# Optimization experiments

Hardware: AMD Instinct MI355X
Metric: run time of the kernel (lower is better)

Reference implementation:

```python
import jax, jax.numpy as jnp
import numpy as np

SC = 19          # window stride/size (non-kitti)
K = 3 * SC       # 57, unfold kernel size
CH = 128         # chnn

def conv2d(x, w, b=None, pad=(0, 0)):
    y = jax.lax.conv_general_dilated(
        x, w, (1, 1), [(pad[0], pad[0]), (pad[1], pad[1])],
        dimension_numbers=('NCHW', 'OIHW', 'NCHW'))
    return y if b is None else y + b[None, :, None, None]

def unfold(x):
    # nn.Unfold(kernel_size=3*SC, padding=SC, stride=SC) -> [b, c, K*K, h_sc*w_sc]
    b, c, h, w = x.shape
    h_sc, w_sc = h // SC, w // SC
    xp = jnp.pad(x, ((0, 0), (0, 0), (SC, SC), (SC, SC)))
    ii = np.arange(h_sc)[:, None] * SC + np.arange(K)[None, :]
    jj = np.arange(w_sc)[:, None] * SC + np.arange(K)[None, :]
    p = xp[:, :, ii, :][:, :, :, :, jj]              # [b,c,h_sc,K,w_sc,K]
    return p.transpose(0, 1, 3, 5, 2, 4).reshape(b, c, K * K, h_sc * w_sc)

def to_windows(x):
    # [b,c,h,w] -> [b,c,h_sc*w_sc, SC*SC] (non-overlapping SCxSC windows)
    b, c, h, w = x.shape
    h_sc, w_sc = h // SC, w // SC
    return x.reshape(b, c, h_sc, SC, w_sc, SC).transpose(0, 1, 2, 4, 3, 5).reshape(b, c, h_sc * w_sc, SC * SC)

def fs_kernel(w_prelu, b, h, w):
    # geometric falloff kernel, separable in x/y: [b, K*K, L, SC*SC]
    a = w_prelu[0] * 0.02      # scp = 0.02
    half = 2.0 * SC            # half_ker
    crd = jnp.arange(K, dtype=jnp.float32)
    idx_x = SC + jnp.arange(w, dtype=jnp.float32) % SC
    idx_y = SC + jnp.arange(h, dtype=jnp.float32) % SC
    def falloff(d):
        v = d - half
        pre = jnp.where(v > 0, v, a * v)   # PReLU
        return jnp.maximum(1.0 - pre, 0.0) # -prelu + b(=1), clamped at 0
    ox = falloff(jnp.abs(crd[:, None] - idx_x[None, :]))  # [K, w]
    oy = falloff(jnp.abs(crd[:, None] - idx_y[None, :]))  # [K, h]
    ker = oy[:, None, :, None] * ox[None, :, None, :]      # [Ky, Kx, h, w]
    ker = jnp.broadcast_to(ker[None], (b, K, K, h, w)).reshape(b, K * K, h, w)
    return to_windows(ker)

def kpa(feat_ci, feat_mi, w_qk, w_v, gamma, w_prelu):
    b, c, h_in, w_in = feat_mi.shape
    x_pad = SC - w_in % SC
    y_pad = SC - h_in % SC
    pad4 = ((0, 0), (0, 0), (0, y_pad), (0, x_pad))
    feat_c = jnp.pad(feat_ci, pad4)
    feat_m = jnp.pad(feat_mi, pad4)
    h, w = h_in + y_pad, w_in + x_pad
    h_sc, w_sc = h // SC, w // SC
    # validity mask -> additive -99 bias for padded keys/queries
    fm = jnp.pad(jnp.ones((1, 1, h_in, w_in), feat_mi.dtype), pad4)
    fm_k = unfold(fm)                                  # [1,1,K^2,L]
    fm_q = to_windows(fm)                              # [1,1,L,SC^2]
    am = (fm_k[:, 0, :, :, None] * fm_q[:, 0, None, :, :] - 1.0) * 99.0
    # itr == 0 path: compute attention
    qk = conv2d(feat_c, w_qk)
    feat_q, feat_k = qk[:, :c], qk[:, c:]
    feat_k = unfold(feat_k) * (c ** -0.5)              # [b,c,K^2,L]
    feat_q = to_windows(feat_q)                        # [b,c,L,SC^2]
    attn = jnp.einsum('bckn,bcns->bkns', feat_k, feat_q) + am
    attn = jax.nn.softmax(fs_kernel(w_prelu, b, h, w) * attn, axis=1)
    feat_v = unfold(conv2d(feat_m, w_v))               # [b,c,K^2,L]
    feat_r = jnp.einsum('bkns,bckn->bcns', attn, feat_v)  # [b,c,L,SC^2]
    feat_r = feat_r.reshape(b, c, h_sc, w_sc, SC, SC).transpose(0, 1, 2, 4, 3, 5).reshape(b, c, h, w)
    return feat_mi + feat_r[:, :, :h_in, :w_in] * gamma[0]

def sep_conv_gru(h, x, wz1, bz1, wr1, br1, wq1, bq1, wz2, bz2, wr2, br2, wq2, bq2):
    hx = jnp.concatenate([h, x], 1)
    z = jax.nn.sigmoid(conv2d(hx, wz1, bz1, (0, 2)))
    r = jax.nn.sigmoid(conv2d(hx, wr1, br1, (0, 2)))
    q = jnp.tanh(conv2d(jnp.concatenate([r * h, x], 1), wq1, bq1, (0, 2)))
    h = (1 - z) * h + z * q
    hx = jnp.concatenate([h, x], 1)
    z = jax.nn.sigmoid(conv2d(hx, wz2, bz2, (2, 0)))
    r = jax.nn.sigmoid(conv2d(hx, wr2, br2, (2, 0)))
    q = jnp.tanh(conv2d(jnp.concatenate([r * h, x], 1), wq2, bq2, (2, 0)))
    return (1 - z) * h + z * q

PARAM_SHAPES = [
    ('w_cor1', (256, 324, 1, 1)), ('b_cor1', (256,)), ('w_cor2', (192, 256, 3, 3)), ('b_cor2', (192,)),
    ('w_flo1', (128, 2, 7, 7)), ('b_flo1', (128,)), ('w_flo2', (64, 128, 3, 3)), ('b_flo2', (64,)),
    ('w_mo', (126, 256, 3, 3)), ('b_mo', (126,)),
    ('w_qk', (256, 128, 1, 1)), ('w_v', (128, 128, 1, 1)),
    ('wz1', (128, 512, 1, 5)), ('bz1', (128,)), ('wr1', (128, 512, 1, 5)), ('br1', (128,)),
    ('wq1', (128, 512, 1, 5)), ('bq1', (128,)),
    ('wz2', (128, 512, 5, 1)), ('bz2', (128,)), ('wr2', (128, 512, 5, 1)), ('br2', (128,)),
    ('wq2', (128, 512, 5, 1)), ('bq2', (128,)),
    ('w_f1', (256, 128, 3, 3)), ('b_f1', (256,)), ('w_f2', (2, 256, 3, 3)), ('b_f2', (2,)),
    ('w_m1', (256, 128, 3, 3)), ('b_m1', (256,)), ('w_m2', (576, 256, 1, 1)), ('b_m2', (576,)),
]

def setup_inputs() -> dict:
    key = jax.random.key(0)
    B, H, W = 2, 55, 128
    ks = jax.random.split(key, len(PARAM_SHAPES) + 4)
    inp = {
        'net': jax.random.normal(ks[0], (B, CH, H, W), jnp.float32),
        'inp': jax.random.normal(ks[1], (B, CH, H, W), jnp.float32),
        'corr': jax.random.normal(ks[2], (B, 324, H, W), jnp.float32),
        'flow': jax.random.normal(ks[3], (B, 2, H, W), jnp.float32),
    }
    for i, (name, shp) in enumerate(PARAM_SHAPES):
        fan_in = int(np.prod(shp[1:])) if len(shp) > 1 else shp[0]
        scale = 1.0 / np.sqrt(fan_in) if len(shp) > 1 else 0.01
        inp[name] = scale * jax.random.normal(ks[4 + i], shp, jnp.float32)
    inp['gamma'] = jnp.array([0.5], jnp.float32)            # nonzero so KPA contributes
    inp['w_prelu'] = jnp.array([1.0 / 28.0], jnp.float32)    # 1 / h_k, h_k = (3*SC-1)/2
    inp['itr'] = 0
    return inp

def reference(net, inp, corr, flow, w_cor1, b_cor1, w_cor2, b_cor2, w_flo1, b_flo1, w_flo2, b_flo2, w_mo, b_mo, w_qk, w_v, wz1, bz1, wr1, br1, wq1, bq1, wz2, bz2, wr2, br2, wq2, bq2, w_f1, b_f1, w_f2, b_f2, w_m1, b_m1, w_m2, b_m2, gamma, w_prelu, itr):
    # _mo_enc
    fc = jax.nn.relu(conv2d(corr, w_cor1, b_cor1))
    fc = jax.nn.relu(conv2d(fc, w_cor2, b_cor2, (1, 1)))
    ff = jax.nn.relu(conv2d(flow, w_flo1, b_flo1, (3, 3)))
    ff = jax.nn.relu(conv2d(ff, w_flo2, b_flo2, (1, 1)))
    fm = jax.nn.relu(conv2d(jnp.concatenate([fc, ff], 1), w_mo, b_mo, (1, 1)))
    feat_mo = jnp.concatenate([fm, flow], 1)           # [b,128,h,w]
    # KPA attention (itr == 0)
    feat_moa = kpa(inp, feat_mo, w_qk, w_v, gamma, w_prelu)
    x = jnp.concatenate([inp, feat_mo, feat_moa], 1)   # [b,384,h,w]
    net = sep_conv_gru(net, x, wz1, bz1, wr1, br1, wq1, bq1, wz2, bz2, wr2, br2, wq2, bq2)
    d = jax.nn.relu(conv2d(net, w_f1, b_f1, (1, 1)))
    delta_flow = conv2d(d, w_f2, b_f2, (1, 1))
    m = jax.nn.relu(conv2d(net, w_m1, b_m1, (1, 1)))
    mask = 0.25 * conv2d(m, w_m2, b_m2)
    return net, mask, delta_flow
```

## Files before the change

kernel.cpp:

```cpp
#include <hip/hip_runtime.h>
#include <hip/hip_bf16.h>

typedef __bf16 bf16;
typedef __attribute__((ext_vector_type(8))) __bf16 v8bf;
typedef __attribute__((ext_vector_type(4))) float f32x4;
typedef __attribute__((ext_vector_type(16))) float f32x16;

#define HH 55
#define WW 128
#define HWP 7040
#define BHW 14080
#define QS 0.08838834764831845f
#define LOG2E 1.4426950408889634f

__device__ __forceinline__ void g2l16(const bf16* g, bf16* l){
  __builtin_amdgcn_global_load_lds(
      (const __attribute__((address_space(1))) void*)g,
      (__attribute__((address_space(3))) void*)l, 16, 0, 0);
}

#define NCV 19
__device__ const int PK_srcCS[NCV]  = {324,256,128,256,128,128,512,512,512,512,512,512,128,128,256,256,98,512,512};
__device__ const int PK_csv[NCV]    = {324,256,128,256,128,128,512,512,128,512,512,128,128,128,256,256,98,384,384};
__device__ const int PK_srcOff[NCV] = {0,0,0,0,0,0,0,0,0,0,0,0,0,0,0,0,0,128,128};
__device__ const int PK_wsrc[NCV]   = {0,1,2,3,4,5,6,7,8,9,10,11,12,13,14,15,16,8,11};
__device__ const int PK_Kc[NCV]     = {384,256,128,256,128,128,512,512,128,512,512,128,128,128,256,256,128,384,384};
__device__ const int PK_ntap[NCV]   = {1,9,9,9,1,1,5,5,5,5,5,5,9,9,9,1,1,5,5};
__device__ const int PK_Ctot[NCV]   = {256,256,128,128,256,128,256,256,128,256,256,128,512,512,128,640,128,128,128};
__device__ const int PK_coB[NCV]    = {0,0,0,0,0,0,0,128,0,0,128,0,0,256,0,0,0,0,0};
__device__ const int PK_dst[NCV]    = {0,98304,688128,835584,1130496,1163264,1179648,1179648,
  1835008,2162688,2162688,2818048,3145728,3145728,3735552,4030464,4194304,1916928,2899968};
__device__ const int PKD_cum[NCV+1] = {0,98304,540672,614400,904704,937472,953856,
  1281536,1609216,1691136,2018816,2346496,2428416,2723328,3018240,3022848,3170304,
  3186688,3432448,3678208};
__device__ const int PKD_Co[NCV]    = {256,192,64,126,256,128,128,128,128,128,128,128,256,256,2,576,128,128,128};

__device__ const int PB_off[15]={0,256,512,640,1152,1280,1408,1536,1664,1792,1920,2176,2432,2560,3200};
__device__ const int PB_cnt[15]={256,192,64,126,128,128,128,128,128,128,256,256,2,576,128};

struct W17 { const float* w[17]; };
struct B15 { const float* b[15]; };

struct XP {
  W17 wp; B15 bp;
  const float *net, *inp, *corr, *flow;
  bf16 *Bp; float *bias;
  bf16 *hx; float *hcur; bf16 *corr_cl; bf16 *im2c;
};

__global__ __launch_bounds__(256) void init_k(XP X){
  __shared__ float T[64][65];
  int bid = blockIdx.x;
  const int t = threadIdx.x;
  if (bid < 14368){
    int idx = bid*256 + t;
    int c = 0;
    while (idx >= PKD_cum[c+1]) ++c;
    int local = idx - PKD_cum[c];
    if (c == 16){
      int co = local >> 7, k = local & 127;
      if (k < 98)
        X.Bp[PK_dst[16] + co*128 + k] = (bf16)X.wp.w[16][co*98 + (k&1)*49 + (k>>1)];
      return;
    }
    int Kc = PK_Kc[c];
    int CKc = PKD_Co[c]*Kc;
    int tap = local / CKc;
    int rem = local - tap*CKc;
    int co = rem / Kc;
    int ci = rem - co*Kc;
    if (ci < PK_csv[c]){
      float v = X.wp.w[PK_wsrc[c]][(co*PK_srcCS[c] + PK_srcOff[c] + ci)*PK_ntap[c] + tap];
      if (c == 4 && co < 128) v *= QS;
      X.Bp[PK_dst[c] + (tap*PK_Ctot[c] + PK_coB[c] + co)*Kc + ci] = (bf16)v;
    }
    return;
  }
  bid -= 14368;
  if (bid < 880){
    int pt = bid%110, ct = (bid/110)&3, b = bid/440;
    const float* src = (ct < 2) ? X.net : X.inp;
    int c0s = (ct & 1)*64;
    int cbase = (ct < 2) ? 0 : 128;
    int p0 = pt*64;
    int pj = t & 63, cr4 = t >> 6;
#pragma unroll
    for (int i=0;i<16;++i)
      T[cr4 + i*4][pj] = src[((size_t)b*128 + c0s + cr4 + i*4)*HWP + p0 + pj];
    __syncthreads();
    int cj = t & 63, pr4 = t >> 6;
#pragma unroll
    for (int i=0;i<16;++i){
      int pp = p0 + pr4 + i*4;
      float v = T[cj][pr4 + i*4];
      X.hx[((size_t)(b*HWP+pp))*512 + cbase + c0s + cj] = (bf16)v;
      if (ct < 2) X.hcur[((size_t)(b*HWP+pp))*128 + c0s + cj] = v;
    }
    return;
  }
  bid -= 880;
  if (bid < 1320){
    int pt = bid%110, ct = (bid/110)%6, b = bid/660;
    int p0 = pt*64, c0s = ct*64;
    int pj = t & 63, cr4 = t >> 6;
#pragma unroll
    for (int i=0;i<16;++i){
      int c = c0s + cr4 + i*4;
      float v = 0.f;
      if (c < 324) v = X.corr[((size_t)b*324 + c)*HWP + p0 + pj];
      T[cr4 + i*4][pj] = v;
    }
    __syncthreads();
    int cj = t & 63, pr4 = t >> 6;
#pragma unroll
    for (int i=0;i<16;++i){
      int pp = p0 + pr4 + i*4;
      int cc = c0s + cj;
      X.corr_cl[((size_t)(b*HWP+pp))*384 + cc] = (bf16)T[cj][pr4 + i*4];
    }
    return;
  }
  bid -= 1320;
  if (bid < 110){
    int i = bid*256 + t;
    int c = i & 1, p = i >> 1;
    int b = p / HWP, pix = p - b*HWP;
    X.hx[(size_t)p*512 + 382 + c] = (bf16)X.flow[(b*2+c)*HWP + pix];
    return;
  }
  bid -= 110;
  if (bid < 7040){
    int i = bid*256 + t;
    int k = i & 127, p = i >> 7;
    int b = p / HWP, pix = p - b*HWP, y = pix >> 7, x = pix & 127;
    float v = 0.f;
    if (k < 98){
      int tap = k >> 1, c2 = k & 1, kh = tap/7, kw = tap - 7*(tap/7);
      int yy = y + kh - 3, xx = x + kw - 3;
      if ((unsigned)yy < 55u && (unsigned)xx < 128u) v = X.flow[(b*2+c2)*HWP + yy*128 + xx];
    }
    X.im2c[i] = (bf16)v;
    return;
  }
  for (int e=0;e<15;++e)
    for (int o=t; o<PB_cnt[e]; o+=256)
      X.bias[PB_off[e]+o] = X.bp.b[e][o];
}

struct GP {
  const bf16* A; const bf16* A2;
  const bf16* Bp; const float* bias;
  void* outp; const float* auxZ; float* auxH; float* auxN; const float* auxQ;
  int Astride, A2stride, Asplit;
  int outCtot, outC0, Nvalid, Kc, CtotPad, tapcode, act, outmode, ntiles, ntOff;
  int ntapN, tapSplit;
  float scale;
};

__global__ __launch_bounds__(256) void gemm_conv(GP ga, GP gb, GP gc, const bf16* __restrict__ zp)
{
  const int Mt = blockIdx.x;
  int nt = blockIdx.y;
  GP g;
  if (nt < ga.ntiles){ g = ga; }
  else if (nt < ga.ntiles + gb.ntiles){ g = gb; nt -= ga.ntiles; }
  else { g = gc; nt -= ga.ntiles + gb.ntiles; }
  int tOff = 0;
  if (g.tapSplit){ tOff = nt * g.ntapN; nt = 0; }
  const bf16* A        = g.A;
  const bf16* A2       = g.A2;
  const bf16* Bp       = g.Bp;
  const float* bias    = g.bias;
  void* outp           = g.outp;
  const float* auxZ    = g.auxZ;
  float* auxH          = g.auxH;
  float* auxN          = g.auxN;
  const float* auxQ    = g.auxQ;
  const int Astride    = g.Astride;
  const int A2stride   = g.A2stride;
  const int Asplit     = g.Asplit;
  const int outCtot    = g.outCtot;
  const int outC0      = g.outC0;
  const int Nvalid     = g.Nvalid;
  const int Kc         = g.Kc;
  const int CtotPad    = g.CtotPad;
  const int tapcode    = g.tapcode;
  const int act        = g.act;
  const int outmode    = g.outmode;
  const int ntOff      = g.ntOff;
  const float scale    = g.scale;

  const int bimg = Mt/110;
  const int rem = Mt - bimg*110;
  const int yy0 = rem >> 1;
  const int xh  = (rem & 1) << 6;
  const int tid = threadIdx.x;
  const int lane = tid & 63, wave = tid >> 6;
  const int wm = wave >> 1, wn = wave & 1;
  const int lr = lane & 15, lq2 = lane >> 4;

  __shared__ __align__(16) bf16 Al[2][4096];
  __shared__ __align__(16) bf16 Bl[2][8192];

  f32x4 acc[2][4];
#pragma unroll
  for (int m=0;m<2;++m)
#pragma unroll
    for (int n=0;n<4;++n) acc[m][n] = (f32x4){0.f,0.f,0.f,0.f};

  const int ntap = g.ntapN ? g.ntapN : ((tapcode==0) ? 1 : (tapcode==1 ? 9 : 5));
  const int nsteps = ntap*(Kc>>6);

  const int srow = tid >> 3;
  const int sc   = tid & 7;

#define STAGE(BUF, T, KC) { \
    int TT = (T) + tOff; \
    int ddy, ddx; \
    if (tapcode==0){ ddy=0; ddx=0; } \
    else if (tapcode==1){ ddy=TT/3-1; ddx=TT-3*(TT/3)-1; } \
    else if (tapcode==2){ ddy=0; ddx=TT-2; } \
    else { ddy=TT-2; ddx=0; } \
    int ysrc = yy0 + ddy; \
    bool yok = (unsigned)ysrc < 55u; \
    const bf16* Abase; int Astr; \
    if ((KC) < Asplit){ Astr = A2stride; \
      Abase = A2 + (size_t)((bimg*55+ysrc)*128)*Astr + (KC); } \
    else { Astr = Astride; \
      Abase = A + (size_t)((bimg*55+ysrc)*128)*Astr + (KC); } \
    _Pragma("unroll") \
    for (int is=0; is<2; ++is){ \
      int r = is*32 + srow; \
      int cc = sc ^ (r&7); \
      int gx = xh + r + ddx; \
      const bf16* srcp = (yok && (unsigned)gx < 128u) ? \
          (Abase + (size_t)gx*Astr + cc*8) : (zp + cc*8); \
      g2l16(srcp, &Al[BUF][is*2048 + wave*512]); \
    } \
    const bf16* Bt = Bp + (size_t)(TT*CtotPad + (nt+ntOff)*128)*Kc + (KC); \
    _Pragma("unroll") \
    for (int is=0; is<4; ++is){ \
      int r = is*32 + srow; \
      int cc = sc ^ (r&7); \
      g2l16(Bt + (size_t)r*Kc + cc*8, &Bl[BUF][is*2048 + wave*512]); \
    } }

  STAGE(0, 0, 0);
  __syncthreads();

  int tcur = 0, kcc = 0;
  for (int si=0; si<nsteps; ++si){
    int kn = kcc + 64, tn = tcur;
    if (kn == Kc){ kn = 0; tn = tcur + 1; }
    if (si + 1 < nsteps){ STAGE((si+1)&1, tn, kn); }
    __builtin_amdgcn_sched_barrier(0);
    kcc = kn; tcur = tn;
    const bf16* Ac = Al[si&1];
    const bf16* Bc = Bl[si&1];
#pragma unroll
    for (int kk=0; kk<2; ++kk){
      v8bf af[2], bfr[4];
#pragma unroll
      for (int m=0;m<2;++m){
        int row = wm*32 + m*16 + lr;
        af[m] = *(const v8bf*)(Ac + row*64 + (((kk*4+lq2) ^ (row&7))<<3));
      }
#pragma unroll
      for (int n=0;n<4;++n){
        int row = wn*64 + n*16 + lr;
        bfr[n] = *(const v8bf*)(Bc + row*64 + (((kk*4+lq2) ^ (row&7))<<3));
      }
#pragma unroll
      for (int m=0;m<2;++m)
#pragma unroll
        for (int n=0;n<4;++n)
          acc[m][n] = __builtin_amdgcn_mfma_f32_16x16x32_bf16(af[m], bfr[n], acc[m][n], 0,0,0);
    }
    __syncthreads();
  }
#undef STAGE

  const size_t pixbase = (size_t)(bimg*55 + yy0)*128 + xh;
  if (outmode == 0){
    bf16* Ost = (bf16*)Al;
#pragma unroll
    for (int nn=0; nn<4; ++nn){
      int colL = wn*64 + nn*16 + lr;
      float bvl = bias[(nt+ntOff)*128 + colL];
#pragma unroll
      for (int m=0;m<2;++m){
        int rowx = wm*32 + m*16 + lq2*4;
        f32x4 v = acc[m][nn];
#pragma unroll
        for (int r=0;r<4;++r){
          float vv = v[r] + bvl;
          if (act==1)      vv = fmaxf(vv, 0.f);
          else if (act==2) vv = 1.f/(1.f+__expf(-vv));
          else if (act==3) vv = tanhf(vv);
          vv *= scale;
          int row = rowx + r;
          int pch = (colL>>3) ^ (row & 7);
          Ost[row*128 + (pch<<3) + (colL&7)] = (bf16)vv;
        }
      }
    }
    __syncthreads();
    {
      int rowl = tid >> 2, seg = tid & 3;
      size_t p = pixbase + rowl;
      bf16* dstp = (bf16*)outp + p*outCtot + outC0 + (nt+ntOff)*128 + seg*32;
      const bf16* srcr = Ost + rowl*128;
      int cb = (nt+ntOff)*128 + seg*32;
#pragma unroll
      for (int k2=0;k2<4;++k2){
        int pch = (seg*4 + k2) ^ (rowl & 7);
        int cog = cb + k2*8;
        if (cog + 8 <= Nvalid)
          *(uint4*)(dstp + k2*8) = *(const uint4*)(srcr + (pch<<3));
        else if (cog < Nvalid){
          const bf16* s8 = srcr + (pch<<3);
          for (int e=0; e<Nvalid-cog; ++e) dstp[k2*8+e] = s8[e];
        }
      }
    }
  } else if (outmode == 2 || outmode == 6){
    float* Ost2 = (float*)Bl;
#pragma unroll
    for (int nn=0; nn<4; ++nn){
      int chL = wn*64 + nn*16 + lr;
      float bvl = (outmode==6 && tOff!=0) ? 0.f : bias[(nt+ntOff)*128 + chL];
#pragma unroll
      for (int m=0;m<2;++m){
        int rowx = wm*32 + m*16 + lq2*4;
        f32x4 v = acc[m][nn];
#pragma unroll
        for (int r=0;r<4;++r){
          float vv = v[r] + bvl;
          if (act==1)      vv = fmaxf(vv, 0.f);
          else if (act==2) vv = 1.f/(1.f+__expf(-vv));
          else if (act==3) vv = tanhf(vv);
          Ost2[chL*64 + rowx + r] = vv*scale;
        }
      }
    }
    __syncthreads();
    {
      int ch = tid >> 1, half = tid & 1;
      int cog = (nt+ntOff)*128 + ch;
      if (cog < Nvalid){
        float* dstp = (float*)outp + ((size_t)bimg*outCtot + outC0 + cog)*HWP
                    + yy0*128 + xh + half*32;
        const float* srcr = Ost2 + ch*64 + half*32;
        if (outmode == 2){
#pragma unroll
          for (int k2=0;k2<8;++k2)
            *(uint4*)(dstp + k2*4) = *(const uint4*)(srcr + k2*4);
        } else {
#pragma unroll
          for (int e=0;e<32;++e)
            atomicAdd(dstp + e, srcr[e]);
        }
      }
    }
  } else if (outmode == 5){
    bf16* Ost3 = (bf16*)Bl;
#pragma unroll
    for (int nn=0; nn<4; ++nn){
      int chL = wn*64 + nn*16 + lr;
      float bvl = bias[(nt+ntOff)*128 + chL];
#pragma unroll
      for (int m=0;m<2;++m){
        int rowx = wm*32 + m*16 + lq2*4;
        f32x4 v = acc[m][nn];
#pragma unroll
        for (int r=0;r<4;++r)
          Ost3[chL*72 + rowx + r] = (bf16)(v[r] + bvl);
      }
    }
    __syncthreads();
    {
      int ch = tid >> 1, half = tid & 1;
      bf16* dstp = (bf16*)outp + ((size_t)bimg*outCtot + outC0 + ch)*HWP
                 + yy0*128 + xh + half*32;
      const bf16* srcr = Ost3 + ch*72 + half*32;
#pragma unroll
      for (int k2=0;k2<4;++k2)
        *(uint4*)(dstp + k2*8) = *(const uint4*)(srcr + k2*8);
    }
  } else {
#pragma unroll
    for (int nn=0; nn<4; ++nn){
      int cog = (nt+ntOff)*128 + wn*64 + nn*16 + lr;
      float bvl = bias[cog];
      bool cok = cog < Nvalid;
#pragma unroll
      for (int m=0;m<2;++m){
        int rowx = wm*32 + m*16 + lq2*4;
        f32x4 v = acc[m][nn];
#pragma unroll
        for (int r=0;r<4;++r){
          int prow = rowx + r;
          size_t p = pixbase + prow;
          float vv = v[r] + bvl;
          if (outmode==4 && auxQ) vv += auxQ[p*128 + cog];
          if (act==1)      vv = fmaxf(vv, 0.f);
          else if (act==2) vv = 1.f/(1.f+__expf(-vv));
          else if (act==3) vv = tanhf(vv);
          vv *= scale;
          if (cok){
            if (outmode==1) ((float*)outp)[p*outCtot + outC0 + cog] = vv;
            else if (outmode==3){
              int c = cog & 127;
              ((bf16*)outp)[p*128 + c] = (bf16)(vv * auxH[p*128 + c]);
            } else {
              int c = cog;
              float z  = auxZ[p*128 + c];
              float h0 = auxH[p*128 + c];
              float hn = (1.f - z)*h0 + z*vv;
              auxH[p*128 + c] = hn;
              ((bf16*)outp)[p*512 + c] = (bf16)hn;
              if (auxN){
                int pixloc = (int)(p - (size_t)bimg*HWP);
                auxN[((size_t)bimg*128 + c)*HWP + pixloc] = hn;
              }
            }
          }
        }
      }
    }
  }
}

__global__ __launch_bounds__(256,1) void attn_k(
    const bf16* __restrict__ QK, const bf16* __restrict__ Vt,
    bf16* __restrict__ hx,
    const float* __restrict__ gammap, const float* __restrict__ wprelup)
{
  __shared__ __align__(16) float SM[16640];
  const int tid = threadIdx.x;
  const int wv = tid >> 6, lane = tid & 63;
  const int lq = lane & 31, hi = lane >> 5;
  const int blk = blockIdx.x;
  const int qt = blk % 12;
  const int n  = (blk/12) % 21;
  const int b  = blk / 252;
  const int hs = n/7, wd = n - 7*hs;
  const int y0 = (hs-1)*19, x0 = (wd-1)*19;
  const int rylo = max(0, y0), ryhi = min(54, y0+56);
  const int rxlo = max(0, x0), rxhi = min(127, x0+56);
  const int rxA  = rxlo & ~7;
  const int s = qt*32 + lq;
  const int sy = s/19, sx = s - sy*19;
  const int qy = y0 + 19 + sy, qx = x0 + 19 + sx;
  const int qpix = (b*55 + min(qy,54))*128 + min(qx,127);
  const float a = wprelup[0]*0.02f;
  const float qyf = (float)qy;

  bf16* Kl = (bf16*)SM + wv*8192;
  bf16* Vl = Kl + 4096;

  v8bf qf[8];
#pragma unroll
  for (int ks=0; ks<8; ++ks)
    qf[ks] = *(const v8bf*)(QK + (size_t)qpix*256 + ks*16 + hi*8);

  float fx0[16], fx1[16];
  unsigned msk0 = 0, msk1 = 0;
  {
    float dxq0 = (float)(rxA - qx);
    int xl0 = rxlo - rxA, xm0 = rxhi - rxA;
#pragma unroll
    for (int r=0;r<16;++r){
      int Ri = (r&3) + 8*(r>>2) + 4*hi;
      float dxv = fabsf(dxq0 + (float)Ri) - 38.f;
      fx0[r] = fmaxf(1.f - fmaxf(dxv, a*dxv), 0.f);
      if (Ri >= xl0 && Ri <= xm0) msk0 |= 1u<<r;
      float dxv1 = fabsf(dxq0 + 32.f + (float)Ri) - 38.f;
      fx1[r] = fmaxf(1.f - fmaxf(dxv1, a*dxv1), 0.f);
      int Ri1 = Ri + 32;
      if (Ri1 >= xl0 && Ri1 <= xm0) msk1 |= 1u<<r;
    }
  }

  f32x16 acc[4];
#pragma unroll
  for (int nf=0; nf<4; ++nf)
#pragma unroll
    for (int r=0;r<16;++r) acc[nf][r] = 0.f;
  float m2 = -40.f, den = 0.f;

  const int nry = (ryhi - rylo - wv)/4 + 1;
  const int nit = nry*2;

#define ISSUE_K(RY, RX) { int pixK = (b*55+(RY))*128 + (RX); \
  _Pragma("unroll") \
  for (int i=0;i<8;++i){ \
    int key = i*4 + (lane>>4); int cs = (lane&15) ^ (key&7); \
    g2l16(QK + (size_t)(pixK+key)*256 + 128 + cs*8, Kl + i*512); } }
#define ISSUE_V(RY, RX) { \
  _Pragma("unroll") \
  for (int i=0;i<8;++i){ \
    int ch = i*16 + (lane>>2); int cs = (lane&3) ^ ((ch>>1)&3); \
    g2l16(Vt + (size_t)(b*128+ch)*HWP + (RY)*128 + (RX) + cs*8, Vl + i*512); } }

  ISSUE_K(rylo + wv, rxA);

  for (int it=0; it<nit; ++it){
    const int ry  = rylo + wv + (it>>1)*4;
    const int tpar = it & 1;
    asm volatile("s_waitcnt lgkmcnt(0)" ::: "memory");
    __builtin_amdgcn_sched_barrier(0);
    asm volatile("s_waitcnt vmcnt(0)" ::: "memory");
    __builtin_amdgcn_sched_barrier(0);
    ISSUE_V(ry, rxA + tpar*32);
    __builtin_amdgcn_sched_barrier(0);

    f32x16 Cs;
#pragma unroll
    for (int r=0;r<16;++r) Cs[r] = 0.f;
#pragma unroll
    for (int ks=0; ks<8; ++ks){
      v8bf kf = *(const v8bf*)(Kl + lq*128 + (((ks*2+hi) ^ (lq&7))<<3));
      Cs = __builtin_amdgcn_mfma_f32_32x32x16_bf16(kf, qf[ks], Cs, 0,0,0);
    }
    float pr[16];
    {
      float dyv = fabsf((float)ry - qyf) - 38.f;
      float fy = fmaxf(1.f - fmaxf(dyv, a*dyv), 0.f);
      float fyk = fy * LOG2E;
      unsigned mk = tpar ? msk1 : msk0;
      float l2v[16]; float tmax = -1e30f;
#pragma unroll
      for (int r=0;r<16;++r){
        float fx = tpar ? fx1[r] : fx0[r];
        float lv = fyk * fx * Cs[r];
        lv = ((mk>>r)&1u) ? lv : -1e30f;
        l2v[r] = lv;
        tmax = fmaxf(tmax, lv);
      }
      tmax = fmaxf(tmax, __shfl_xor(tmax, 32));
      if (__any(tmax > m2 + 11.f)){
        float m2n = fmaxf(m2, tmax);
        float sc = exp2f(m2 - m2n);
        den *= sc;
#pragma unroll
        for (int r=0;r<16;++r){
          float scr = __shfl(sc, (r&3) + 8*(r>>2) + 4*hi);
          acc[0][r]*=scr; acc[1][r]*=scr; acc[2][r]*=scr; acc[3][r]*=scr;
        }
        m2 = m2n;
      }
#pragma unroll
      for (int r=0;r<16;++r){
        pr[r] = exp2f(l2v[r] - m2);
        den += pr[r];
      }
    }
    asm volatile("s_waitcnt lgkmcnt(0)" ::: "memory");
    __builtin_amdgcn_sched_barrier(0);
    asm volatile("s_waitcnt vmcnt(0)" ::: "memory");
    __builtin_amdgcn_sched_barrier(0);
    if (it + 1 < nit){
      int ryn = rylo + wv + ((it+1)>>1)*4;
      ISSUE_K(ryn, rxA + ((it+1)&1)*32);
      __builtin_amdgcn_sched_barrier(0);
    }
    unsigned w0,w1,w2,w3,w4,w5,w6,w7;
    asm("v_cvt_pk_bf16_f32 %0, %1, %2" : "=v"(w0) : "v"(pr[0]),  "v"(pr[1]));
    asm("v_cvt_pk_bf16_f32 %0, %1, %2" : "=v"(w1) : "v"(pr[2]),  "v"(pr[3]));
    asm("v_cvt_pk_bf16_f32 %0, %1, %2" : "=v"(w2) : "v"(pr[4]),  "v"(pr[5]));
    asm("v_cvt_pk_bf16_f32 %0, %1, %2" : "=v"(w3) : "v"(pr[6]),  "v"(pr[7]));
    asm("v_cvt_pk_bf16_f32 %0, %1, %2" : "=v"(w4) : "v"(pr[8]),  "v"(pr[9]));
    asm("v_cvt_pk_bf16_f32 %0, %1, %2" : "=v"(w5) : "v"(pr[10]), "v"(pr[11]));
    asm("v_cvt_pk_bf16_f32 %0, %1, %2" : "=v"(w6) : "v"(pr[12]), "v"(pr[13]));
    asm("v_cvt_pk_bf16_f32 %0, %1, %2" : "=v"(w7) : "v"(pr[14]), "v"(pr[15]));
    asm("v_permlane32_swap_b32 %0, %1" : "+v"(w0), "+v"(w2));
    asm("v_permlane32_swap_b32 %0, %1" : "+v"(w1), "+v"(w3));
    asm("v_permlane32_swap_b32 %0, %1" : "+v"(w4), "+v"(w6));
    asm("v_permlane32_swap_b32 %0, %1" : "+v"(w5), "+v"(w7));
    union { unsigned u[4]; v8bf v; } U0, U1;
    U0.u[0]=w0; U0.u[1]=w1; U0.u[2]=w2; U0.u[3]=w3;
    U1.u[0]=w4; U1.u[1]=w5; U1.u[2]=w6; U1.u[3]=w7;
    v8bf pa0 = U0.v, pa1 = U1.v;
#pragma unroll
    for (int nf=0; nf<4; ++nf){
      int ch = nf*32 + lq;
      int sw = (lq>>1)&3;
      v8bf v0 = *(const v8bf*)(Vl + ch*32 + ((hi     ^ sw)<<3));
      v8bf v1 = *(const v8bf*)(Vl + ch*32 + (((2+hi) ^ sw)<<3));
      acc[nf] = __builtin_amdgcn_mfma_f32_32x32x16_bf16(pa0, v0, acc[nf], 0,0,0);
      acc[nf] = __builtin_amdgcn_mfma_f32_32x32x16_bf16(pa1, v1, acc[nf], 0,0,0);
    }
  }
#undef ISSUE_K
#undef ISSUE_V
  den += __shfl_xor(den, 32);

  float* Osh = SM;
  float* Msh = SM + 16384;
  float* Dsh = SM + 16512;
  __syncthreads();
#pragma unroll
  for (int nf=0; nf<4; ++nf)
#pragma unroll
    for (int r=0;r<16;++r)
      Osh[(wv*32 + (r&3) + 8*(r>>2) + 4*hi)*128 + nf*32 + lq] = acc[nf][r];
  if (hi == 0){ Msh[wv*32 + lq] = m2; Dsh[wv*32 + lq] = den; }
  __syncthreads();

  int q = tid >> 3, co = (tid & 7)*16;
  float m0 = Msh[q], m1 = Msh[32+q], mm2 = Msh[64+q], m3 = Msh[96+q];
  float M = fmaxf(fmaxf(m0,m1), fmaxf(mm2,m3));
  float s0 = exp2f(m0-M), s1 = exp2f(m1-M), s2 = exp2f(mm2-M), s3 = exp2f(m3-M);
  int ss = qt*32 + q;
  float dent = s0*Dsh[q] + s1*Dsh[32+q] + s2*Dsh[64+q] + s3*Dsh[96+q];
  int sy2 = ss/19, sx2 = ss - sy2*19;
  int qy2 = y0 + 19 + sy2, qx2 = x0 + 19 + sx2;
  if (ss < 361 && qy2 < 55 && qx2 < 128){
    size_t pix = (size_t)(b*55+qy2)*128 + qx2;
    float g = gammap[0] / dent;
    v8bf fm0 = *(const v8bf*)(hx + pix*512 + 256 + co);
    v8bf fm1 = *(const v8bf*)(hx + pix*512 + 256 + co + 8);
    v8bf o0, o1;
#pragma unroll
    for (int c=0;c<8;++c){
      float oa = s0*Osh[q*128+co+c] + s1*Osh[(32+q)*128+co+c]
               + s2*Osh[(64+q)*128+co+c] + s3*Osh[(96+q)*128+co+c];
      o0[c] = (bf16)((float)fm0[c] + oa*g);
      float ob = s0*Osh[q*128+co+8+c] + s1*Osh[(32+q)*128+co+8+c]
               + s2*Osh[(64+q)*128+co+8+c] + s3*Osh[(96+q)*128+co+8+c];
      o1[c] = (bf16)((float)fm1[c] + ob*g);
    }
    *(v8bf*)(hx + pix*512 + 384 + co)     = o0;
    *(v8bf*)(hx + pix*512 + 384 + co + 8) = o1;
  }
}

static inline GP mkgp(const bf16* A, int Astride, const bf16* Bp, const float* bias,
                      void* outp, int outCtot, int outC0, int Nvalid, int Kc, int CtotPad,
                      int tapcode, int act, int outmode, float scale, int ntiles){
  GP g{};
  g.A=A; g.A2=A; g.Astride=Astride; g.A2stride=Astride; g.Asplit=0;
  g.Bp=Bp; g.bias=bias; g.outp=outp;
  g.auxZ=nullptr; g.auxH=nullptr; g.auxN=nullptr; g.auxQ=nullptr;
  g.outCtot=outCtot; g.outC0=outC0; g.Nvalid=Nvalid; g.Kc=Kc; g.CtotPad=CtotPad;
  g.tapcode=tapcode; g.act=act; g.outmode=outmode; g.ntiles=ntiles; g.ntOff=0;
  g.ntapN=0; g.tapSplit=0;
  g.scale=scale;
  return g;
}

extern "C" void kernel_launch(void* const* d_in, const int* in_sizes, int n_in,
                              void* d_out, int out_size, void* d_ws, size_t ws_size,
                              hipStream_t stream) {
  const float* net   = (const float*)d_in[0];
  const float* inp   = (const float*)d_in[1];
  const float* corr  = (const float*)d_in[2];
  const float* flow  = (const float*)d_in[3];
  const float* w_cor1=(const float*)d_in[4];  const float* b_cor1=(const float*)d_in[5];
  const float* w_cor2=(const float*)d_in[6];  const float* b_cor2=(const float*)d_in[7];
  const float* w_flo1=(const float*)d_in[8];  const float* b_flo1=(const float*)d_in[9];
  const float* w_flo2=(const float*)d_in[10]; const float* b_flo2=(const float*)d_in[11];
  const float* w_mo  =(const float*)d_in[12]; const float* b_mo  =(const float*)d_in[13];
  const float* w_qk  =(const float*)d_in[14];
  const float* w_v   =(const float*)d_in[15];
  const float* wz1=(const float*)d_in[16]; const float* bz1=(const float*)d_in[17];
  const float* wr1=(const float*)d_in[18]; const float* br1=(const float*)d_in[19];
  const float* wq1=(const float*)d_in[20]; const float* bq1=(const float*)d_in[21];
  const float* wz2=(const float*)d_in[22]; const float* bz2=(const float*)d_in[23];
  const float* wr2=(const float*)d_in[24]; const float* br2=(const float*)d_in[25];
  const float* wq2=(const float*)d_in[26]; const float* bq2=(const float*)d_in[27];
  const float* w_f1=(const float*)d_in[28]; const float* b_f1=(const float*)d_in[29];
  const float* w_f2=(const float*)d_in[30]; const float* b_f2=(const float*)d_in[31];
  const float* w_m1=(const float*)d_in[32]; const float* b_m1=(const float*)d_in[33];
  const float* w_m2=(const float*)d_in[34]; const float* b_m2=(const float*)d_in[35];
  const float* gamma  =(const float*)d_in[36];
  const float* w_prelu=(const float*)d_in[37];

  float* ws = (float*)d_ws;
  bf16* hx     = (bf16*)ws;
  bf16* BPp    = (bf16*)(ws + 3604480);
  float* BIASp = ws + 5709824;
  const bf16* zp = (const bf16*)(ws + 5713152);
  float* ZB0   = ws + 5713216;
  const size_t S0 = 5713344;
  bf16* corr_cl = (bf16*)(ws + S0);
  bf16* fc1o    = (bf16*)(ws + S0 + 2703360);
  bf16* catB    = (bf16*)(ws + S0 + 4505600);
  bf16* ff1o    = (bf16*)(ws + S0 + 6307840);
  bf16* im2c    = (bf16*)(ws + S0 + 7208960);
  float* hcur   = ws + S0 + 8110080;
  bf16* QKb    = (bf16*)(ws + S0);
  bf16* Vt     = (bf16*)(ws + S0 + 2711552);
  float* zb    = ws + S0;
  float* qpart = ws + S0 + 1802240;
  bf16* rhb    = (bf16*)(ws + S0 + 3604480);
  bf16* dm     = (bf16*)(ws + S0);

  float* out_net  = (float*)d_out;
  float* out_mask = out_net + 1802240;
  float* out_df   = out_net + 9912320;

  dim3 blk(256);

  hipMemsetAsync(ws + 3604480, 0, (size_t)8435456, stream);
  hipMemsetAsync(out_df, 0, (size_t)28160*sizeof(float), stream);
  XP X{};
  const float* wl[17] = {w_cor1,w_cor2,w_flo2,w_mo,w_qk,w_v,wz1,wr1,wq1,wz2,wr2,wq2,w_f1,w_m1,w_f2,w_m2,w_flo1};
  const float* bl[15] = {b_cor1,b_cor2,b_flo2,b_mo,bz1,br1,bq1,bz2,br2,bq2,b_f1,b_m1,b_f2,b_m2,b_flo1};
  for (int i=0;i<17;++i) X.wp.w[i]=wl[i];
  for (int i=0;i<15;++i) X.bp.b[i]=bl[i];
  X.net=net; X.inp=inp; X.corr=corr; X.flow=flow;
  X.Bp=BPp; X.bias=BIASp; X.hx=hx; X.hcur=hcur; X.corr_cl=corr_cl; X.im2c=im2c;
  init_k<<<dim3(14368+880+1320+110+7040+1),blk,0,stream>>>(X);

  GP g0{};

  {
    GP a = mkgp(corr_cl,384, BPp+0,       BIASp+0,    fc1o,256,0,256, 384,256, 0,1,0,1.f, 2);
    GP b = mkgp(im2c,128,    BPp+4194304, BIASp+3200, ff1o,128,0,128, 128,128, 0,1,0,1.f, 1);
    gemm_conv<<<dim3(220,3),blk,0,stream>>>(a, b, g0, zp);
  }
  {
    GP a = mkgp(fc1o,256,    BPp+98304,   BIASp+256,  catB,256,0,192, 256,256, 1,1,0,1.f, 2);
    GP b = mkgp(ff1o,128,    BPp+688128,  BIASp+512,  catB,256,192,64,128,128, 1,1,0,1.f, 1);
    gemm_conv<<<dim3(220,3),blk,0,stream>>>(a, b, g0, zp);
  }

  {
    GP a = mkgp(catB,256,    BPp+835584,  BIASp+640,  hx,  512,256,126,256,128, 1,1,0,1.f, 1);
    GP b = mkgp(hx+128,512,  BPp+1130496, BIASp+768,  QKb, 256,0,256, 128,256, 0,0,0,1.f, 2);
    gemm_conv<<<dim3(220,3),blk,0,stream>>>(a, b, g0, zp);
  }
  {
    GP a = mkgp(hx+256,512,  BPp+1163264, BIASp+1024, Vt,  128,0,128, 128,128, 0,0,5,1.f, 1);
    gemm_conv<<<dim3(220,1),blk,0,stream>>>(a, g0, g0, zp);
  }
  attn_k<<<dim3(504),blk,0,stream>>>(QKb, Vt, hx, gamma, w_prelu);

  {
    GP a = mkgp(hx,512,      BPp+1179648, BIASp+1152, zb,  128,0,128, 512,256, 2,2,1,1.f, 1);
    GP b = mkgp(hx,512,      BPp+1179648, BIASp+1152, rhb, 0,0,256,   512,256, 2,2,3,1.f, 1);
    b.ntOff = 1; b.auxH = hcur;
    GP c = mkgp(hx+128,512,  BPp+1916928, ZB0,        qpart,128,0,128,384,128, 2,0,1,1.f, 1);
    gemm_conv<<<dim3(220,3),blk,0,stream>>>(a, b, c, zp);
  }
  {
    GP a = mkgp(rhb,128,     BPp+1835008, BIASp+1408, hx,  0,0,128,   128,128, 2,3,4,1.f, 1);
    a.auxZ = zb; a.auxH = hcur; a.auxN = nullptr; a.auxQ = qpart;
    gemm_conv<<<dim3(220,1),blk,0,stream>>>(a, g0, g0, zp);
  }

  {
    GP a = mkgp(hx,512,      BPp+2162688, BIASp+1536, zb,  128,0,128, 512,256, 3,2,1,1.f, 1);
    GP b = mkgp(hx,512,      BPp+2162688, BIASp+1536, rhb, 0,0,256,   512,256, 3,2,3,1.f, 1);
    b.ntOff = 1; b.auxH = hcur;
    GP c = mkgp(hx+128,512,  BPp+2899968, ZB0,        qpart,128,0,128,384,128, 3,0,1,1.f, 1);
    gemm_conv<<<dim3(220,3),blk,0,stream>>>(a, b, c, zp);
  }
  {
    GP a = mkgp(rhb,128,     BPp+2818048, BIASp+1792, hx,  0,0,128,   128,128, 3,3,4,1.f, 1);
    a.auxZ = zb; a.auxH = hcur; a.auxN = out_net; a.auxQ = qpart;
    gemm_conv<<<dim3(220,1),blk,0,stream>>>(a, g0, g0, zp);
  }

  {
    GP a = mkgp(hx,512,      BPp+3145728, BIASp+1920, dm,  512,0,512, 128,512, 1,1,0,1.f, 4);
    gemm_conv<<<dim3(220,4),blk,0,stream>>>(a, g0, g0, zp);
  }
  {
    GP a = mkgp(dm+256,512,  BPp+4030464, BIASp+2560, out_mask,576,0,576,256,640, 0,0,2,0.25f, 5);
    GP b = mkgp(dm,512,      BPp+3735552, BIASp+2432, out_df,  2,  0,2,  256,128, 1,0,6,1.f,   3);
    b.tapSplit = 1; b.ntapN = 3;
    gemm_conv<<<dim3(220,8),blk,0,stream>>>(a, b, g0, zp);
  }
}
```

Baseline: 488.5 us.

## Split mo-conv GEMM over taps with fp32 atomic staging and merge kernel

The 3x3 conv producing the motion features (catB -> hx) is now split across three tap groups (tapSplit, outmode 6), which raises its grid from one N-tile column to three and accumulates partial sums into a zeroed fp32 staging buffer. A new merge_k kernel transposes that staging buffer through shared memory, applies ReLU, converts to bf16 and writes into hx while keeping the existing flow channels in the last vector. This adds more parallel blocks to an under-occupied launch, at the cost of an extra memset, an extra kernel launch and fp32 atomic or staging traffic.

Result: slower. 751.2 us (+53.8%).

```diff
diff --git a/kernel.cpp b/kernel.cpp
--- a/kernel.cpp
+++ b/kernel.cpp
@@ -145,6 +145,40 @@
   for (int e=0;e<15;++e)
     for (int o=t; o<PB_cnt[e]; o+=256)
       X.bias[PB_off[e]+o] = X.bp.b[e][o];
+}
+
+__global__ __launch_bounds__(256) void merge_k(
+    const float* __restrict__ stag, bf16* __restrict__ hx)
+{
+  __shared__ float T[128][65];
+  const int Mt = blockIdx.x;
+  const int bimg = Mt/110;
+  const int rem = Mt - bimg*110;
+  const int pixloc0 = (rem>>1)*128 + ((rem & 1) << 6);
+  const int t = threadIdx.x;
+#pragma unroll
+  for (int it=0; it<32; ++it){
+    int idx = t + it*256;
+    int ch = idx >> 6, px = idx & 63;
+    T[ch][px] = stag[((size_t)bimg*128 + ch)*HWP + pixloc0 + px];
+  }
+  __syncthreads();
+  const int px = t >> 2, seg = t & 3;
+  const size_t hbase = ((size_t)bimg*HWP + pixloc0 + px)*512 + 256;
+#pragma unroll
+  for (int k=0;k<4;++k){
+    int c0 = seg*32 + k*8;
+    v8bf o;
+    if (c0 == 120){
+      o = *(const v8bf*)(hx + hbase + 120);
+#pragma unroll
+      for (int e=0;e<6;++e) o[e] = (bf16)fmaxf(T[120+e][px], 0.f);
+    } else {
+#pragma unroll
+      for (int e=0;e<8;++e) o[e] = (bf16)fmaxf(T[c0+e][px], 0.f);
+    }
+    *(v8bf*)(hx + hbase + c0) = o;
+  }
 }
 
 struct GP {
@@ -686,6 +720,7 @@
   const size_t S0 = 5713344;
   bf16* corr_cl = (bf16*)(ws + S0);
   bf16* fc1o    = (bf16*)(ws + S0 + 2703360);
+  float* fc1oF  = ws + S0 + 2703360;
   bf16* catB    = (bf16*)(ws + S0 + 4505600);
   bf16* ff1o    = (bf16*)(ws + S0 + 6307840);
   bf16* im2c    = (bf16*)(ws + S0 + 7208960);
@@ -727,11 +762,15 @@
     gemm_conv<<<dim3(220,3),blk,0,stream>>>(a, b, g0, zp);
   }
 
-  {
-    GP a = mkgp(catB,256,    BPp+835584,  BIASp+640,  hx,  512,256,126,256,128, 1,1,0,1.f, 1);
+  hipMemsetAsync(fc1oF, 0, (size_t)7208960, stream);
+  {
+    GP a = mkgp(catB,256,    BPp+835584,  BIASp+640,  fc1oF,128,0,126,256,128, 1,0,6,1.f, 3);
+    a.tapSplit = 1; a.ntapN = 3;
     GP b = mkgp(hx+128,512,  BPp+1130496, BIASp+768,  QKb, 256,0,256, 128,256, 0,0,0,1.f, 2);
-    gemm_conv<<<dim3(220,3),blk,0,stream>>>(a, b, g0, zp);
-  }
+    gemm_conv<<<dim3(220,5),blk,0,stream>>>(a, b, g0, zp);
+  }
+  merge_k<<<dim3(220),blk,0,stream>>>(fc1oF, hx);
+
   {
     GP a = mkgp(hx+256,512,  BPp+1163264, BIASp+1024, Vt,  128,0,128, 128,128, 0,0,5,1.f, 1);
     gemm_conv<<<dim3(220,1),blk,0,stream>>>(a, g0, g0, zp);
```
